# Optimization experiments

Measured on AMD Instinct MI355X. Metric: run time of the kernel, lower is better.

## Reference

```python
import jax, jax.numpy as jnp
import numpy as np

NUM_EDGES = 10000
NUM_PATHS = 30000
MAX_LEN = 16
LINK_DIM = 128
PATH_DIM = 128


def setup_inputs() -> dict:
    key = jax.random.key(0)
    k0, k1, k2, k3, k4, k5, k6, k7 = jax.random.split(key, 8)
    inputs = jax.random.normal(k0, (NUM_EDGES, LINK_DIM), dtype=jnp.float32)
    # every path has exactly MAX_LEN hops -> unique (path, pos) scatter indices
    idx = jnp.repeat(jnp.arange(NUM_PATHS, dtype=jnp.int64), MAX_LEN)
    seqs = jnp.tile(jnp.arange(MAX_LEN, dtype=jnp.int64), NUM_PATHS)
    paths = jax.random.randint(k1, (NUM_PATHS * MAX_LEN,), 0, NUM_EDGES).astype(jnp.int64)
    # GRU params (Keras GRUCell, reset_after=True): kernel [D,3U], recurrent [U,3U], two bias rows
    s_in = 1.0 / np.sqrt(LINK_DIM)
    s_h = 1.0 / np.sqrt(PATH_DIM)
    kernel = jax.random.uniform(k2, (LINK_DIM, 3 * PATH_DIM), minval=-s_in, maxval=s_in, dtype=jnp.float32)
    rec_kernel = jax.random.uniform(k3, (PATH_DIM, 3 * PATH_DIM), minval=-s_h, maxval=s_h, dtype=jnp.float32)
    bias_i = jnp.zeros((3 * PATH_DIM,), dtype=jnp.float32)
    bias_r = jnp.zeros((3 * PATH_DIM,), dtype=jnp.float32)
    wq = jax.random.uniform(k4, (PATH_DIM, PATH_DIM), minval=-s_h, maxval=s_h, dtype=jnp.float32)
    wk = jax.random.uniform(k5, (PATH_DIM, PATH_DIM), minval=-s_h, maxval=s_h, dtype=jnp.float32)
    wv = jax.random.uniform(k6, (PATH_DIM, PATH_DIM), minval=-s_h, maxval=s_h, dtype=jnp.float32)
    return {"inputs": inputs, "paths": paths, "idx": idx, "seqs": seqs,
            "kernel": kernel, "rec_kernel": rec_kernel, "bias_i": bias_i, "bias_r": bias_r,
            "wq": wq, "wk": wk, "wv": wv}


def _gru_scan(link_inputs, kernel, rec_kernel, bias_i, bias_r):
    # link_inputs: [P, L, D] -> hidden_states [P, L, U], last_state [P, U]
    U = rec_kernel.shape[0]
    P = link_inputs.shape[0]
    xs = jnp.transpose(link_inputs, (1, 0, 2))  # [L, P, D]

    def step(h, x):
        xm = x @ kernel + bias_i          # [P, 3U]
        hm = h @ rec_kernel + bias_r      # [P, 3U]  (reset_after=True)
        xz, xr, xh = xm[:, :U], xm[:, U:2 * U], xm[:, 2 * U:]
        hz, hr, hh = hm[:, :U], hm[:, U:2 * U], hm[:, 2 * U:]
        z = jax.nn.sigmoid(xz + hz)
        r = jax.nn.sigmoid(xr + hr)
        cand = jnp.tanh(xh + r * hh)
        h_new = z * h + (1.0 - z) * cand
        return h_new, h_new

    h0 = jnp.zeros((P, U), dtype=link_inputs.dtype)
    last, hs = jax.lax.scan(step, h0, xs)
    return jnp.transpose(hs, (1, 0, 2)), last  # [P, L, U], [P, U]


def reference(inputs, paths, idx, seqs, kernel, rec_kernel, bias_i, bias_r, wq, wk, wv):
    h_tild = inputs[paths]  # gather: [P*L, D]
    link_inputs = jnp.zeros((NUM_PATHS, MAX_LEN, LINK_DIM), dtype=inputs.dtype)
    link_inputs = link_inputs.at[idx, seqs].set(h_tild)  # scatter_nd
    hidden_states, last_state = _gru_scan(link_inputs, kernel, rec_kernel, bias_i, bias_r)
    key = jnp.einsum('plu,uv->plv', hidden_states, wk)
    query = last_state @ wq                     # [P, U]
    value = jnp.einsum('plu,uv->plv', hidden_states, wv)
    att = jnp.einsum('plv,pv->pl', key, query)  # raw scores, no softmax (faithful)
    context = jnp.einsum('pl,plv->pv', att, value)[:, None, :]  # [P, 1, U]
    return context
```

## Files before the change

### kernel.cpp

```cpp
#include <hip/hip_runtime.h>


#define NUM_PATHS 30000
#define T 16
#define NTILES 1875
#define NEDGES 10000

#define SC1 1.4426950408889634f
#define SC2 2.8853900817779268f

typedef float f32x4 __attribute__((ext_vector_type(4)));
typedef short bf16x8 __attribute__((ext_vector_type(8)));
typedef short bf16x4 __attribute__((ext_vector_type(4)));

__device__ __forceinline__ short f2bf(float f) {
    union { float f; unsigned u; } v; v.f = f;
    return (short)((v.u + 0x8000u) >> 16);
}
__device__ __forceinline__ float bf2f(short s) {
    union { unsigned u; float f; } v; v.u = ((unsigned)(unsigned short)s) << 16;
    return v.f;
}
__device__ __forceinline__ float vexp2(float x) {
    float r; asm("v_exp_f32 %0, %1" : "=v"(r) : "v"(x)); return r;
}
__device__ __forceinline__ float vexp2n(float x) {
    float r; asm("v_exp_f32 %0, -%1" : "=v"(r) : "v"(x)); return r;
}

#define MFMA(a, b, c) __builtin_amdgcn_mfma_f32_16x16x32_bf16((a), (b), (c), 0, 0, 0)

#define GRU_T 12288
#define QK_T 16384
#define WV_T 2048
__global__ void prep_kernel(const float* __restrict__ Wx, const float* __restrict__ Wr,
                            const float* __restrict__ wq, const float* __restrict__ wk,
                            const float* __restrict__ wv,
                            short* __restrict__ wpk) {
    int id = blockIdx.x * 256 + threadIdx.x;
    if (id < GRU_T) {
        int f = id >> 9, rem = id & 511;
        int w = rem >> 6, lane = rem & 63;
        int quad = lane >> 4, c16 = lane & 15;
        int col = 16 * w + c16;
        short o[8];
        #pragma unroll
        for (int j = 0; j < 8; ++j) {
            float v;
            if (f < 16) {
                int k = (f & 7) * 32 + quad * 8 + j;
                int cc = col + ((f < 8) ? 0 : 128);
                v = ((k < 128) ? Wx[k * 384 + cc] : Wr[(k - 128) * 384 + cc]) * SC1;
            } else {
                int k = ((f - 16) & 3) * 32 + quad * 8 + j;
                v = ((f < 20) ? Wx[k * 384 + 256 + col] : Wr[k * 384 + 256 + col]) * SC2;
            }
            o[j] = f2bf(v);
        }
        *(bf16x8*)&wpk[id * 8] = *(bf16x8*)o;
        return;
    }
    if (id < GRU_T + QK_T) {
        int t2 = id - GRU_T;
        int j = t2 & 7, lane = (t2 >> 3) & 63, w = (t2 >> 9) & 7, kc = t2 >> 12;
        int quad = lane >> 4, c16 = lane & 15, col = 16 * w + c16;
        int k = kc * 32 + quad * 8 + j;
        const float* qr = wq + k * 128;
        const float* kr = wk + col * 128;
        float s = 0.f;
        #pragma unroll 8
        for (int vv = 0; vv < 128; ++vv) s += qr[vv] * kr[vv];
        short hi = f2bf(s);
        wpk[(((24 + kc) * 8 + w) * 64 + lane) * 8 + j] = hi;
        wpk[(((28 + kc) * 8 + w) * 64 + lane) * 8 + j] = f2bf(s - bf2f(hi));
        return;
    }
    if (id < GRU_T + QK_T + WV_T) {
        int t2 = id - GRU_T - QK_T;
        int lane = t2 & 63, w = (t2 >> 6) & 7, kc = t2 >> 9;
        int quad = lane >> 4, c16 = lane & 15, col = 16 * w + c16;
        short hi8[8], lo8[8];
        #pragma unroll
        for (int j = 0; j < 8; ++j) {
            float v = wv[(kc * 32 + quad * 8 + j) * 128 + col];
            hi8[j] = f2bf(v);
            lo8[j] = f2bf(v - bf2f(hi8[j]));
        }
        *(bf16x8*)&wpk[(((32 + kc) * 8 + w) * 64 + lane) * 8] = *(bf16x8*)hi8;
        *(bf16x8*)&wpk[(((36 + kc) * 8 + w) * 64 + lane) * 8] = *(bf16x8*)lo8;
    }
}

__global__ __launch_bounds__(512) void eprep_kernel(
    const float* __restrict__ inputs, const short* __restrict__ wpk,
    const float* __restrict__ bias_i, uint2* __restrict__ E8) {
    const int w = threadIdx.x >> 6, lane = threadIdx.x & 63;
    const int quad = lane >> 4, c16 = lane & 15;
    const int ucol = 16 * w + c16;
    const int e0 = blockIdx.x * 16;

    const float bxh = bias_i[256 + ucol] * SC2;

    bf16x8 A[4];
    const float* row = inputs + (e0 + c16) * 128;
    #pragma unroll
    for (int kc = 0; kc < 4; ++kc) {
        float4 a = *(const float4*)&row[kc * 32 + quad * 8];
        float4 b = *(const float4*)&row[kc * 32 + quad * 8 + 4];
        short o[8] = {f2bf(a.x), f2bf(a.y), f2bf(a.z), f2bf(a.w),
                      f2bf(b.x), f2bf(b.y), f2bf(b.z), f2bf(b.w)};
        A[kc] = *(bf16x8*)o;
    }
    f32x4 az = {0.f, 0.f, 0.f, 0.f}, ar = az, ax = az;
    #pragma unroll
    for (int kc = 0; kc < 4; ++kc) {
        bf16x8 Bz = *(const bf16x8*)&wpk[(((0 + kc) * 8 + w) * 64 + lane) * 8];
        bf16x8 Br = *(const bf16x8*)&wpk[(((8 + kc) * 8 + w) * 64 + lane) * 8];
        bf16x8 Bx = *(const bf16x8*)&wpk[(((16 + kc) * 8 + w) * 64 + lane) * 8];
        az = MFMA(A[kc], Bz, az);
        ar = MFMA(A[kc], Br, ar);
        ax = MFMA(A[kc], Bx, ax);
    }
    #pragma unroll
    for (int r = 0; r < 4; ++r) {
        unsigned zr = (unsigned)(unsigned short)f2bf(az[r]) |
                      ((unsigned)(unsigned short)f2bf(ar[r]) << 16);
        uint2 val;
        val.x = zr;
        val.y = __float_as_uint(ax[r] + bxh);
        E8[(e0 + quad * 4 + r) * 128 + ucol] = val;
    }
}

#define ROWS 136
#define HSLOT 2184

__global__ __launch_bounds__(512, 4) void path_emb_kernel(
    const int* __restrict__ paths, const short* __restrict__ wpk,
    const uint2* __restrict__ E8,
    const float* __restrict__ bias_i, const float* __restrict__ bias_r,
    float* __restrict__ out)
{
    __shared__ __align__(16) short s_hist[16][HSLOT];
    __shared__ __align__(16) short s_xb[2][T * ROWS];
    __shared__ float s_att[16][20];

    const int tid  = threadIdx.x;
    const int w    = tid >> 6;
    const int lane = tid & 63;
    const int quad = lane >> 4;
    const int c16  = lane & 15;
    const int ucol = 16 * w + c16;

    const float bz  = (bias_i[ucol] + bias_r[ucol]) * SC1;
    const float brr = (bias_i[128 + ucol] + bias_r[128 + ucol]) * SC1;
    const float bhh = bias_r[256 + ucol] * SC2;

    bf16x8 Bzh[4], Brh[4], Bhh[4];
    #pragma unroll
    for (int kc = 0; kc < 4; ++kc) {
        Bzh[kc] = *(const bf16x8*)&wpk[(((4 + kc)  * 8 + w) * 64 + lane) * 8];
        Brh[kc] = *(const bf16x8*)&wpk[(((12 + kc) * 8 + w) * 64 + lane) * 8];
        Bhh[kc] = *(const bf16x8*)&wpk[(((20 + kc) * 8 + w) * 64 + lane) * 8];
    }

    const int p0 = blockIdx.x * T;

    float hA[4] = {0.f, 0.f, 0.f, 0.f};

    const int* pbase = paths + (p0 + quad * 4) * 16;
    const uint2* Erow = E8 + ucol;

    uint2 Ea[4], Eb[4], Ec[4];

    {
        int id0[4], id1[4];
        #pragma unroll
        for (int i = 0; i < 4; ++i) id0[i] = pbase[i * 16 + 0];
        #pragma unroll
        for (int i = 0; i < 4; ++i) id1[i] = pbase[i * 16 + 1];
        #pragma unroll
        for (int i = 0; i < 4; ++i) Ea[i] = Erow[id0[i] * 128];
        #pragma unroll
        for (int i = 0; i < 4; ++i) Eb[i] = Erow[id1[i] * 128];
    }

    auto window = [&](int t, uint2* Ecur, uint2* Enxt) {
        __syncthreads();

        if (t < 14) {
            int en[4];
            #pragma unroll
            for (int i = 0; i < 4; ++i)
                en[i] = pbase[i * 16 + t + 2];
            #pragma unroll
            for (int i = 0; i < 4; ++i) Enxt[i] = Erow[en[i] * 128];
        }

        f32x4 az  = {bz, bz, bz, bz};
        f32x4 ar  = {brr, brr, brr, brr};
        f32x4 ach = {bhh, bhh, bhh, bhh};

        if (t > 0) {
            bf16x8 ah[4];
            #pragma unroll
            for (int kc = 0; kc < 4; ++kc)
                ah[kc] = *(const bf16x8*)&s_hist[t - 1][c16 * ROWS + kc * 32 + quad * 8];
            __builtin_amdgcn_s_setprio(1);
            #pragma unroll
            for (int kc = 0; kc < 4; ++kc) {
                az  = MFMA(ah[kc], Bzh[kc], az);
                ar  = MFMA(ah[kc], Brh[kc], ar);
                ach = MFMA(ah[kc], Bhh[kc], ach);
            }
            __builtin_amdgcn_s_setprio(0);
        }

        #pragma unroll
        for (int r = 0; r < 4; ++r) {
            uint2 Ec_ = Ecur[r];
            float zx = __uint_as_float(Ec_.x << 16);
            float rx = __uint_as_float(Ec_.x & 0xffff0000u);
            float xh = __uint_as_float(Ec_.y);
            float z    = __builtin_amdgcn_rcpf(1.0f + vexp2n(az[r] + zx));
            float rr   = __builtin_amdgcn_rcpf(1.0f + vexp2n(ar[r] + rx));
            float e2   = vexp2(xh + rr * ach[r]);
            float cand = 1.0f - 2.0f * __builtin_amdgcn_rcpf(1.0f + e2);
            hA[r] = cand + z * (hA[r] - cand);
            s_hist[t][(quad * 4 + r) * ROWS + ucol] = f2bf(hA[r]);
        }
    };

    #pragma unroll 1
    for (int t3 = 0; t3 < 5; ++t3) {
        window(3 * t3 + 0, Ea, Ec);
        window(3 * t3 + 1, Eb, Ea);
        window(3 * t3 + 2, Ec, Eb);
    }
    window(15, Ea, Ec);

    #pragma unroll
    for (int r = 0; r < 4; ++r) {
        float hf = hA[r]; short hi = f2bf(hf);
        s_xb[0][(quad * 4 + r) * ROWS + ucol] = f2bf(hf - bf2f(hi));
    }
    __syncthreads();

    f32x4 uA = {0.f, 0.f, 0.f, 0.f};
    #pragma unroll
    for (int kc = 0; kc < 4; ++kc) {
        bf16x8 bqh = *(const bf16x8*)&wpk[(((24 + kc) * 8 + w) * 64 + lane) * 8];
        bf16x8 bql = *(const bf16x8*)&wpk[(((28 + kc) * 8 + w) * 64 + lane) * 8];
        bf16x8 Ah  = *(const bf16x8*)&s_hist[15][c16 * ROWS + kc * 32 + quad * 8];
        bf16x8 Al  = *(const bf16x8*)&s_xb[0][c16 * ROWS + kc * 32 + quad * 8];
        uA = MFMA(Ah, bqh, uA); uA = MFMA(Ah, bql, uA); uA = MFMA(Al, bqh, uA);
    }
    __syncthreads();

    #pragma unroll
    for (int r = 0; r < 4; ++r) {
        int off = (quad * 4 + r) * ROWS + ucol;
        float v = uA[r]; short hi = f2bf(v);
        s_xb[0][off] = hi; s_xb[1][off] = f2bf(v - bf2f(hi));
    }
    __syncthreads();

    {
        bf16x8 Uh[4], Ul[4];
        #pragma unroll
        for (int kc = 0; kc < 4; ++kc) {
            Uh[kc] = *(const bf16x8*)&s_xb[0][c16 * ROWS + kc * 32 + quad * 8];
            Ul[kc] = *(const bf16x8*)&s_xb[1][c16 * ROWS + kc * 32 + quad * 8];
        }
        #pragma unroll
        for (int li = 0; li < 2; ++li) {
            int l = 2 * w + li;
            f32x4 acc = {0.f, 0.f, 0.f, 0.f};
            #pragma unroll
            for (int kc = 0; kc < 4; ++kc) {
                bf16x8 Bh = *(const bf16x8*)&s_hist[l][c16 * ROWS + kc * 32 + quad * 8];
                acc = MFMA(Uh[kc], Bh, acc);
                acc = MFMA(Ul[kc], Bh, acc);
            }
            float d01 = (c16 & 1) ? acc[1] : acc[0];
            float d23 = (c16 & 1) ? acc[3] : acc[2];
            float dv  = (c16 & 2) ? d23 : d01;
            if (quad == (c16 >> 2)) s_att[c16][l] = dv;
        }
    }
    __syncthreads();

    {
        int p = tid >> 5, c0 = (tid & 31) * 4;
        float ctx[4] = {0.f, 0.f, 0.f, 0.f};
        #pragma unroll
        for (int l = 0; l < 16; ++l) {
            float al = s_att[p][l];
            bf16x4 hv = *(const bf16x4*)&s_hist[l][p * ROWS + c0];
            #pragma unroll
            for (int j = 0; j < 4; ++j) ctx[j] += al * bf2f(hv[j]);
        }
        #pragma unroll
        for (int j = 0; j < 4; ++j) {
            short hi = f2bf(ctx[j]);
            s_xb[0][p * ROWS + c0 + j] = hi;
            s_xb[1][p * ROWS + c0 + j] = f2bf(ctx[j] - bf2f(hi));
        }
    }
    __syncthreads();

    f32x4 oA = {0.f, 0.f, 0.f, 0.f};
    #pragma unroll
    for (int kc = 0; kc < 4; ++kc) {
        bf16x8 bwh = *(const bf16x8*)&wpk[(((32 + kc) * 8 + w) * 64 + lane) * 8];
        bf16x8 bwl = *(const bf16x8*)&wpk[(((36 + kc) * 8 + w) * 64 + lane) * 8];
        bf16x8 Ah  = *(const bf16x8*)&s_xb[0][c16 * ROWS + kc * 32 + quad * 8];
        bf16x8 Al  = *(const bf16x8*)&s_xb[1][c16 * ROWS + kc * 32 + quad * 8];
        oA = MFMA(Ah, bwh, oA); oA = MFMA(Ah, bwl, oA); oA = MFMA(Al, bwh, oA);
    }
    #pragma unroll
    for (int r = 0; r < 4; ++r)
        out[(p0 + quad * 4 + r) * 128 + ucol] = oA[r];
}

extern "C" void kernel_launch(void* const* d_in, const int* in_sizes, int n_in,
                              void* d_out, int out_size, void* d_ws, size_t ws_size,
                              hipStream_t stream) {
    const float* inputs = (const float*)d_in[0];
    const int*   paths  = (const int*)d_in[1];
    const float* wx  = (const float*)d_in[4];
    const float* wr  = (const float*)d_in[5];
    const float* bi  = (const float*)d_in[6];
    const float* br  = (const float*)d_in[7];
    const float* wq  = (const float*)d_in[8];
    const float* wk  = (const float*)d_in[9];
    const float* wvp = (const float*)d_in[10];

    char* ws = (char*)d_ws;
    uint2* E8 = (uint2*)ws;
    short* wpk = (short*)(ws + 10240000);

    int prep_n = GRU_T + QK_T + WV_T;
    prep_kernel<<<(prep_n + 255) / 256, 256, 0, stream>>>(wx, wr, wq, wk, wvp, wpk);
    eprep_kernel<<<NEDGES / 16, 512, 0, stream>>>(inputs, wpk, bi, E8);
    path_emb_kernel<<<NTILES, 512, 0, stream>>>(paths, wpk, E8, bi, br, (float*)d_out);
}
```

Before: 193.7 us.

## Transpose recurrent GRU MFMA so each lane owns contiguous hidden units, vectorize gathers

Swaps the MFMA operand roles in the recurrent step so each lane holds 4 contiguous hidden units of one path rather than 4 paths at one unit. This lets each lane gather its E8 row with two 16-byte loads instead of four scattered 8-byte loads, and store the new hidden state to shared memory as one packed write using a hardware bf16 pack instruction. The z/r biases are folded into the precomputed edge table to remove per-step bias setup. The risk is that changing fragment ownership breaks the later attention stage's indexing, and that bf16 rounding of the folded biases alters numerics slightly.

```diff
diff --git a/kernel.cpp b/kernel.cpp
--- a/kernel.cpp
+++ b/kernel.cpp
@@ -26,6 +26,10 @@
 }
 __device__ __forceinline__ float vexp2n(float x) {
     float r; asm("v_exp_f32 %0, -%1" : "=v"(r) : "v"(x)); return r;
+}
+__device__ __forceinline__ unsigned cvtpk(float a, float b) {
+    unsigned r; asm("v_cvt_pk_bf16_f32 %0, %1, %2" : "=v"(r) : "v"(a), "v"(b));
+    return r;
 }
 
 #define MFMA(a, b, c) __builtin_amdgcn_mfma_f32_16x16x32_bf16((a), (b), (c), 0, 0, 0)
@@ -93,13 +97,16 @@
 
 __global__ __launch_bounds__(512) void eprep_kernel(
     const float* __restrict__ inputs, const short* __restrict__ wpk,
-    const float* __restrict__ bias_i, uint2* __restrict__ E8) {
+    const float* __restrict__ bias_i, const float* __restrict__ bias_r,
+    uint2* __restrict__ E8) {
     const int w = threadIdx.x >> 6, lane = threadIdx.x & 63;
     const int quad = lane >> 4, c16 = lane & 15;
     const int ucol = 16 * w + c16;
     const int e0 = blockIdx.x * 16;
 
     const float bxh = bias_i[256 + ucol] * SC2;
+    const float bzc = (bias_i[ucol] + bias_r[ucol]) * SC1;
+    const float brc = (bias_i[128 + ucol] + bias_r[128 + ucol]) * SC1;
 
     bf16x8 A[4];
     const float* row = inputs + (e0 + c16) * 128;
@@ -123,8 +130,8 @@
     }
     #pragma unroll
     for (int r = 0; r < 4; ++r) {
-        unsigned zr = (unsigned)(unsigned short)f2bf(az[r]) |
-                      ((unsigned)(unsigned short)f2bf(ar[r]) << 16);
+        unsigned zr = (unsigned)(unsigned short)f2bf(az[r] + bzc) |
+                      ((unsigned)(unsigned short)f2bf(ar[r] + brc) << 16);
         uint2 val;
         val.x = zr;
         val.y = __float_as_uint(ax[r] + bxh);
@@ -151,98 +158,106 @@
     const int quad = lane >> 4;
     const int c16  = lane & 15;
     const int ucol = 16 * w + c16;
-
-    const float bz  = (bias_i[ucol] + bias_r[ucol]) * SC1;
-    const float brr = (bias_i[128 + ucol] + bias_r[128 + ucol]) * SC1;
-    const float bhh = bias_r[256 + ucol] * SC2;
-
-    bf16x8 Bzh[4], Brh[4], Bhh[4];
-    #pragma unroll
-    for (int kc = 0; kc < 4; ++kc) {
-        Bzh[kc] = *(const bf16x8*)&wpk[(((4 + kc)  * 8 + w) * 64 + lane) * 8];
-        Brh[kc] = *(const bf16x8*)&wpk[(((12 + kc) * 8 + w) * 64 + lane) * 8];
-        Bhh[kc] = *(const bf16x8*)&wpk[(((20 + kc) * 8 + w) * 64 + lane) * 8];
-    }
+    const int d0   = 16 * w + quad * 4;
+
+    bf16x8 Azh[4], Arh[4], Ahh[4];
+    #pragma unroll
+    for (int kc = 0; kc < 4; ++kc) {
+        Azh[kc] = *(const bf16x8*)&wpk[(((4 + kc)  * 8 + w) * 64 + lane) * 8];
+        Arh[kc] = *(const bf16x8*)&wpk[(((12 + kc) * 8 + w) * 64 + lane) * 8];
+        Ahh[kc] = *(const bf16x8*)&wpk[(((20 + kc) * 8 + w) * 64 + lane) * 8];
+    }
+
+    f32x4 bhv;
+    {
+        float4 b4 = *(const float4*)&bias_r[256 + d0];
+        bhv[0] = b4.x * SC2; bhv[1] = b4.y * SC2;
+        bhv[2] = b4.z * SC2; bhv[3] = b4.w * SC2;
+    }
+    f32x4 ZV = {0.f, 0.f, 0.f, 0.f};
 
     const int p0 = blockIdx.x * T;
 
     float hA[4] = {0.f, 0.f, 0.f, 0.f};
 
-    const int* pbase = paths + (p0 + quad * 4) * 16;
-    const uint2* Erow = E8 + ucol;
-
-    uint2 Ea[4], Eb[4], Ec[4];
-
-    {
-        int id0[4], id1[4];
-        #pragma unroll
-        for (int i = 0; i < 4; ++i) id0[i] = pbase[i * 16 + 0];
-        #pragma unroll
-        for (int i = 0; i < 4; ++i) id1[i] = pbase[i * 16 + 1];
-        #pragma unroll
-        for (int i = 0; i < 4; ++i) Ea[i] = Erow[id0[i] * 128];
-        #pragma unroll
-        for (int i = 0; i < 4; ++i) Eb[i] = Erow[id1[i] * 128];
-    }
-
-    auto window = [&](int t, uint2* Ecur, uint2* Enxt) {
+    const int* pb = paths + (p0 + c16) * 16;
+    const uint2* Ebase = E8 + d0;
+
+    uint4 Ea0, Ea1, Eb0, Eb1, Ec0, Ec1;
+    {
+        int i0 = pb[0], i1 = pb[1];
+        const uint4* e0p = (const uint4*)(Ebase + (size_t)i0 * 128);
+        const uint4* e1p = (const uint4*)(Ebase + (size_t)i1 * 128);
+        Ea0 = e0p[0]; Ea1 = e0p[1];
+        Eb0 = e1p[0]; Eb1 = e1p[1];
+    }
+
+    #define GATE(r, ZR, XH) {                                                  \
+        float zx = __uint_as_float((ZR) << 16);                                \
+        float rx = __uint_as_float((ZR) & 0xffff0000u);                        \
+        float xh = __uint_as_float(XH);                                        \
+        float z    = __builtin_amdgcn_rcpf(1.0f + vexp2n(az[r] + zx));         \
+        float rr   = __builtin_amdgcn_rcpf(1.0f + vexp2n(ar[r] + rx));         \
+        float e2   = vexp2(xh + rr * ach[r]);                                  \
+        float cand = 1.0f - 2.0f * __builtin_amdgcn_rcpf(1.0f + e2);           \
+        hA[r] = cand + z * (hA[r] - cand); }
+
+    auto window = [&](int t, uint4& c0, uint4& c1, uint4& n0, uint4& n1) {
         __syncthreads();
 
         if (t < 14) {
-            int en[4];
-            #pragma unroll
-            for (int i = 0; i < 4; ++i)
-                en[i] = pbase[i * 16 + t + 2];
-            #pragma unroll
-            for (int i = 0; i < 4; ++i) Enxt[i] = Erow[en[i] * 128];
-        }
-
-        f32x4 az  = {bz, bz, bz, bz};
-        f32x4 ar  = {brr, brr, brr, brr};
-        f32x4 ach = {bhh, bhh, bhh, bhh};
+            int en = pb[t + 2];
+            const uint4* ep = (const uint4*)(Ebase + (size_t)en * 128);
+            n0 = ep[0]; n1 = ep[1];
+        }
+
+        f32x4 az = ZV, ar = ZV, ach = bhv;
 
         if (t > 0) {
-            bf16x8 ah[4];
+            bf16x8 bh[4];
             #pragma unroll
             for (int kc = 0; kc < 4; ++kc)
-                ah[kc] = *(const bf16x8*)&s_hist[t - 1][c16 * ROWS + kc * 32 + quad * 8];
+                bh[kc] = *(const bf16x8*)&s_hist[t - 1][c16 * ROWS + kc * 32 + quad * 8];
             __builtin_amdgcn_s_setprio(1);
             #pragma unroll
             for (int kc = 0; kc < 4; ++kc) {
-                az  = MFMA(ah[kc], Bzh[kc], az);
-                ar  = MFMA(ah[kc], Brh[kc], ar);
-                ach = MFMA(ah[kc], Bhh[kc], ach);
+                az  = MFMA(Azh[kc], bh[kc], az);
+                ar  = MFMA(Arh[kc], bh[kc], ar);
+                ach = MFMA(Ahh[kc], bh[kc], ach);
             }
             __builtin_amdgcn_s_setprio(0);
         }
 
-        #pragma unroll
-        for (int r = 0; r < 4; ++r) {
-            uint2 Ec_ = Ecur[r];
-            float zx = __uint_as_float(Ec_.x << 16);
-            float rx = __uint_as_float(Ec_.x & 0xffff0000u);
-            float xh = __uint_as_float(Ec_.y);
-            float z    = __builtin_amdgcn_rcpf(1.0f + vexp2n(az[r] + zx));
-            float rr   = __builtin_amdgcn_rcpf(1.0f + vexp2n(ar[r] + rx));
-            float e2   = vexp2(xh + rr * ach[r]);
-            float cand = 1.0f - 2.0f * __builtin_amdgcn_rcpf(1.0f + e2);
-            hA[r] = cand + z * (hA[r] - cand);
-            s_hist[t][(quad * 4 + r) * ROWS + ucol] = f2bf(hA[r]);
-        }
+        GATE(0, c0.x, c0.y)
+        GATE(1, c0.z, c0.w)
+        GATE(2, c1.x, c1.y)
+        GATE(3, c1.z, c1.w)
+
+        uint2 pk;
+        pk.x = cvtpk(hA[0], hA[1]);
+        pk.y = cvtpk(hA[2], hA[3]);
+        *(uint2*)&s_hist[t][c16 * ROWS + d0] = pk;
     };
 
     #pragma unroll 1
     for (int t3 = 0; t3 < 5; ++t3) {
-        window(3 * t3 + 0, Ea, Ec);
-        window(3 * t3 + 1, Eb, Ea);
-        window(3 * t3 + 2, Ec, Eb);
-    }
-    window(15, Ea, Ec);
-
-    #pragma unroll
-    for (int r = 0; r < 4; ++r) {
-        float hf = hA[r]; short hi = f2bf(hf);
-        s_xb[0][(quad * 4 + r) * ROWS + ucol] = f2bf(hf - bf2f(hi));
+        window(3 * t3 + 0, Ea0, Ea1, Ec0, Ec1);
+        window(3 * t3 + 1, Eb0, Eb1, Ea0, Ea1);
+        window(3 * t3 + 2, Ec0, Ec1, Eb0, Eb1);
+    }
+    window(15, Ea0, Ea1, Ec0, Ec1);
+
+    {
+        unsigned q0 = cvtpk(hA[0], hA[1]);
+        unsigned q1 = cvtpk(hA[2], hA[3]);
+        float l0 = hA[0] - bf2f((short)(q0 & 0xffffu));
+        float l1 = hA[1] - bf2f((short)(q0 >> 16));
+        float l2 = hA[2] - bf2f((short)(q1 & 0xffffu));
+        float l3 = hA[3] - bf2f((short)(q1 >> 16));
+        uint2 rk;
+        rk.x = cvtpk(l0, l1);
+        rk.y = cvtpk(l2, l3);
+        *(uint2*)&s_xb[0][c16 * ROWS + d0] = rk;
     }
     __syncthreads();
 
@@ -342,6 +357,6 @@
 
     int prep_n = GRU_T + QK_T + WV_T;
     prep_kernel<<<(prep_n + 255) / 256, 256, 0, stream>>>(wx, wr, wq, wk, wvp, wpk);
-    eprep_kernel<<<NEDGES / 16, 512, 0, stream>>>(inputs, wpk, bi, E8);
+    eprep_kernel<<<NEDGES / 16, 512, 0, stream>>>(inputs, wpk, bi, br, E8);
     path_emb_kernel<<<NTILES, 512, 0, stream>>>(paths, wpk, E8, bi, br, (float*)d_out);
 }
```

Result: slower. 205.4 us (+6.0%).
